# Performance work log

Measured on AMD Instinct MI355X. Metric: run time of the kernel, lower is better.

## Reference

```python
import jax, jax.numpy as jnp
import numpy as np

N = 65536
NUM_NODES = 100000
NUM_SAMPLED = 16
EMB = 128


def setup_inputs() -> dict:
    key = jax.random.key(0)
    k1, k2, k3, k4, k5 = jax.random.split(key, 5)
    inputs = {
        "input": jax.random.normal(k1, (N,), dtype=jnp.float32),
        "embs": jax.random.normal(k2, (N, EMB), dtype=jnp.float32),
        "label": jax.random.randint(k3, (N,), 0, NUM_NODES),
        "negs": jax.random.randint(k4, (N, NUM_SAMPLED), 0, NUM_NODES),
        # weights initialized ~ N(0, 1/sqrt(emb)) as in reset_parameters
        "weights": jax.random.normal(k5, (NUM_NODES, EMB), dtype=jnp.float32)
        * (1.0 / np.sqrt(EMB)),
    }
    return inputs


def reference(input, embs, label, negs, weights):
    n = input.shape[0]
    # positive term: log(sigmoid(<embs_i, weights[label_i]>))
    pos_score = jnp.sum(embs * weights[label], axis=1)  # [n]
    log_target = jax.nn.log_sigmoid(pos_score)
    # negative term: noise = -weights[negs]; bmm(noise, embs) -> [n, num_sampled]
    neg_score = -jnp.einsum("nkd,nd->nk", weights[negs], embs)
    sum_log_sampled = jnp.sum(jax.nn.log_sigmoid(neg_score), axis=1)  # [n]
    loss = log_target + sum_log_sampled
    return -jnp.sum(loss) / n
```

## Files before the change

### kernel.cpp

```cpp
#include <hip/hip_runtime.h>

#define NROWS 65536
#define EMB 128
#define NS 16
#define NUM_NODES 100000
#define HALF_NODE 50000
#define NB (NROWS / 16)
#define NB_F32 (NROWS / 16)

#define QSTEP 0.0296101f
#define QSTEP_INV 33.7722f
#define ESCALE 23.0f
#define SCALE (QSTEP / ESCALE)

__device__ __forceinline__ float log_sigmoid(float x) {
    return fminf(x, 0.0f) - __logf(1.0f + __expf(-fabsf(x)));
}

__device__ __forceinline__ int sdot4_sw(unsigned a, unsigned b, int c) {
#pragma unroll
    for (int i = 0; i < 4; ++i) {
        int ai = (int)(a << (24 - 8 * i)) >> 24;
        int bi = (int)(b << (24 - 8 * i)) >> 24;
        c += ai * bi;
    }
    return c;
}
#if defined(__has_builtin)
#if __has_builtin(__builtin_amdgcn_sdot4)
#define SDOT4(a, b, c) __builtin_amdgcn_sdot4((int)(a), (int)(b), (c), false)
#endif
#endif
#ifndef SDOT4
#define SDOT4(a, b, c) sdot4_sw((a), (b), (c))
#endif

#define DOTB(P, PE, PO, OUT)                                   \
    {                                                          \
        unsigned _b0 = (P) & 0x0F0F0F0Fu;                      \
        unsigned _b1 = ((P) >> 4) & 0x0F0F0F0Fu;               \
        OUT = SDOT4(_b1, (PO), SDOT4(_b0, (PE), 0));           \
    }

#define BFLYI(OUT, LO, HI, B, MASK)                   \
    {                                                 \
        int _k = (B) ? (HI) : (LO);                   \
        int _s = (B) ? (LO) : (HI);                   \
        OUT = _k + __shfl_xor(_s, (MASK), 64);        \
    }

__device__ __forceinline__ int qe8(float x) {
    int v = (int)rintf(x * ESCALE);
    return v < -127 ? -127 : (v > 127 ? 127 : v);
}

__global__ __launch_bounds__(256) void convert_w_i4(
    const float* __restrict__ w, unsigned int* __restrict__ out, int n8)
{
    int i = blockIdx.x * blockDim.x + threadIdx.x;
    if (i < n8) {
        const float4* p4 = (const float4*)(w + (size_t)i * 8);
        float4 a = p4[0], b = p4[1];
        float v[8] = {a.x, a.y, a.z, a.w, b.x, b.y, b.z, b.w};
        unsigned int p = 0;
#pragma unroll
        for (int j = 0; j < 8; ++j) {
            int n = (int)rintf(v[j] * QSTEP_INV);
            n = n < -7 ? -7 : (n > 7 ? 7 : n);
            p |= ((unsigned int)(n + 8)) << (4 * j);
        }
        out[i] = p;
    }
}

__device__ __forceinline__ float row_term_par(
    int row, int q, unsigned pbit,
    const int* __restrict__ label,
    const int* __restrict__ negs,
    const unsigned* __restrict__ wq,
    unsigned pe, unsigned po, int es)
{
    const int lab = label[row];
    const int4* ng = (const int4*)negs + (unsigned)row * 4u;
    const int4 n0 = ng[0], n1 = ng[1], n2 = ng[2], n3 = ng[3];

#define OWN(IDX) ((unsigned)((IDX) >= HALF_NODE) == pbit)
#define GATHER(IDX) (OWN(IDX) ? wq[(unsigned)(IDX) * 16u + (unsigned)q] : 0u)
    const unsigned wp0  = GATHER(n0.x), wp1  = GATHER(n0.y);
    const unsigned wp2  = GATHER(n0.z), wp3  = GATHER(n0.w);
    const unsigned wp4  = GATHER(n1.x), wp5  = GATHER(n1.y);
    const unsigned wp6  = GATHER(n1.z), wp7  = GATHER(n1.w);
    const unsigned wp8  = GATHER(n2.x), wp9  = GATHER(n2.y);
    const unsigned wp10 = GATHER(n2.z), wp11 = GATHER(n2.w);
    const unsigned wp12 = GATHER(n3.x), wp13 = GATHER(n3.y);
    const unsigned wp14 = GATHER(n3.z), wp15 = GATHER(n3.w);
    const unsigned wpp  = GATHER(lab);
#undef GATHER

    int a0, a1, a2, a3, a4, a5, a6, a7, a8, a9, a10, a11, a12, a13, a14, a15, posi;
    DOTB(wp0,  pe, po, a0);   DOTB(wp1,  pe, po, a1);
    DOTB(wp2,  pe, po, a2);   DOTB(wp3,  pe, po, a3);
    DOTB(wp4,  pe, po, a4);   DOTB(wp5,  pe, po, a5);
    DOTB(wp6,  pe, po, a6);   DOTB(wp7,  pe, po, a7);
    DOTB(wp8,  pe, po, a8);   DOTB(wp9,  pe, po, a9);
    DOTB(wp10, pe, po, a10);  DOTB(wp11, pe, po, a11);
    DOTB(wp12, pe, po, a12);  DOTB(wp13, pe, po, a13);
    DOTB(wp14, pe, po, a14);  DOTB(wp15, pe, po, a15);
    DOTB(wpp,  pe, po, posi);

    const bool b0 = (q & 1), b1 = (q & 2), b2 = (q & 4), b3 = (q & 8);
    int s10, s11, s12, s13, s14, s15, s16, s17;
    BFLYI(s10, a0,  a1,  b0, 1);  BFLYI(s11, a2,  a3,  b0, 1);
    BFLYI(s12, a4,  a5,  b0, 1);  BFLYI(s13, a6,  a7,  b0, 1);
    BFLYI(s14, a8,  a9,  b0, 1);  BFLYI(s15, a10, a11, b0, 1);
    BFLYI(s16, a12, a13, b0, 1);  BFLYI(s17, a14, a15, b0, 1);
    int s20, s21, s22, s23;
    BFLYI(s20, s10, s11, b1, 2);  BFLYI(s21, s12, s13, b1, 2);
    BFLYI(s22, s14, s15, b1, 2);  BFLYI(s23, s16, s17, b1, 2);
    int s30, s31;
    BFLYI(s30, s20, s21, b2, 4);  BFLYI(s31, s22, s23, b2, 4);
    int mynegi;
    BFLYI(mynegi, s30, s31, b3, 8);

    posi += __shfl_xor(posi, 1, 64);
    posi += __shfl_xor(posi, 2, 64);
    posi += __shfl_xor(posi, 4, 64);
    posi += __shfl_xor(posi, 8, 64);

    int mi = n0.x;
    mi = (q == 1)  ? n0.y : mi;  mi = (q == 2)  ? n0.z : mi;
    mi = (q == 3)  ? n0.w : mi;  mi = (q == 4)  ? n1.x : mi;
    mi = (q == 5)  ? n1.y : mi;  mi = (q == 6)  ? n1.z : mi;
    mi = (q == 7)  ? n1.w : mi;  mi = (q == 8)  ? n2.x : mi;
    mi = (q == 9)  ? n2.y : mi;  mi = (q == 10) ? n2.z : mi;
    mi = (q == 11) ? n2.w : mi;  mi = (q == 12) ? n3.x : mi;
    mi = (q == 13) ? n3.y : mi;  mi = (q == 14) ? n3.z : mi;
    mi = (q == 15) ? n3.w : mi;

    const int corr = es << 3;
    const float myneg = (float)(mynegi - corr) * SCALE;
    const float pos   = (float)(posi   - corr) * SCALE;

    float c = OWN(mi) ? log_sigmoid(-myneg) : 0.0f;
    if (q == 0 && OWN(lab)) c += log_sigmoid(pos);
#undef OWN

    c += __shfl_xor(c, 1, 64);
    c += __shfl_xor(c, 2, 64);
    c += __shfl_xor(c, 4, 64);
    c += __shfl_xor(c, 8, 64);
    return c;
}

__global__ __launch_bounds__(256) void nsloss_partial_i4(
    const float*        __restrict__ embs,
    const int*          __restrict__ label,
    const int*          __restrict__ negs,
    const unsigned int* __restrict__ wq,
    float*              __restrict__ partial)
{
    const int tid = threadIdx.x;
    const int q   = tid & 15;
    const int g   = tid >> 4;
    const unsigned bid  = blockIdx.x;
    const unsigned pbit = bid & 1u;
    const int base = (int)(bid >> 1) * 32;

    const float4* e8 = (const float4*)embs;
    float c = 0.0f;

#pragma unroll
    for (int rr = 0; rr < 2; ++rr) {
        const int row = base + rr * 16 + g;
        const unsigned eb4 = (unsigned)row * 32u;
        const float4 ea = e8[eb4 + 2u * q];
        const float4 eb = e8[eb4 + 2u * q + 1u];
        const int q0 = qe8(ea.x), q1 = qe8(ea.y), q2 = qe8(ea.z), q3 = qe8(ea.w);
        const int q4 = qe8(eb.x), q5 = qe8(eb.y), q6 = qe8(eb.z), q7 = qe8(eb.w);
        const unsigned pe = (unsigned)(q0 & 255) | ((unsigned)(q2 & 255) << 8) |
                            ((unsigned)(q4 & 255) << 16) | ((unsigned)(q6 & 255) << 24);
        const unsigned po = (unsigned)(q1 & 255) | ((unsigned)(q3 & 255) << 8) |
                            ((unsigned)(q5 & 255) << 16) | ((unsigned)(q7 & 255) << 24);
        int es = SDOT4(0x01010101u, pe, SDOT4(0x01010101u, po, 0));
        es += __shfl_xor(es, 1, 64);
        es += __shfl_xor(es, 2, 64);
        es += __shfl_xor(es, 4, 64);
        es += __shfl_xor(es, 8, 64);

        c += row_term_par(row, q, pbit, label, negs, wq, pe, po, es);
    }

    __shared__ float s[16];
    if (q == 0) s[g] = c;
    __syncthreads();
    if (tid == 0) {
        float t = 0.0f;
#pragma unroll
        for (int i = 0; i < 16; ++i) t += s[i];
        partial[bid] = t;
    }
}

__device__ __forceinline__ float dot8f(float4 a0, float4 a1, float4 b0, float4 b1) {
    return a0.x * b0.x + a0.y * b0.y + a0.z * b0.z + a0.w * b0.w +
           a1.x * b1.x + a1.y * b1.y + a1.z * b1.z + a1.w * b1.w;
}

__global__ __launch_bounds__(256) void nsloss_partial_f32(
    const float* __restrict__ embs,
    const int*   __restrict__ label,
    const int*   __restrict__ negs,
    const float* __restrict__ weights,
    float*       __restrict__ partial)
{
    const int tid = threadIdx.x;
    const int q   = tid & 15;
    const int row = blockIdx.x * 16 + (tid >> 4);

    const float4* e4 = (const float4*)(embs + (size_t)row * EMB);
    const float4 e0 = e4[q];
    const float4 e1 = e4[q + 16];

    const int lab = label[row];
    const int4* ng = (const int4*)(negs + (size_t)row * NS);
    const int4 n0 = ng[0], n1 = ng[1], n2 = ng[2], n3 = ng[3];
    const int nidx[NS] = {n0.x, n0.y, n0.z, n0.w, n1.x, n1.y, n1.z, n1.w,
                          n2.x, n2.y, n2.z, n2.w, n3.x, n3.y, n3.z, n3.w};

    float acc[NS + 1];
    {
        const float4* w4 = (const float4*)(weights + (size_t)lab * EMB);
        acc[NS] = dot8f(e0, e1, w4[q], w4[q + 16]);
    }
#pragma unroll
    for (int k = 0; k < NS; ++k) {
        const float4* w4 = (const float4*)(weights + (size_t)nidx[k] * EMB);
        acc[k] = dot8f(e0, e1, w4[q], w4[q + 16]);
    }

#pragma unroll
    for (int k = 0; k < NS + 1; ++k) {
        acc[k] += __shfl_xor(acc[k], 1, 64);
        acc[k] += __shfl_xor(acc[k], 2, 64);
        acc[k] += __shfl_xor(acc[k], 4, 64);
        acc[k] += __shfl_xor(acc[k], 8, 64);
    }

    float myneg = 0.0f;
#pragma unroll
    for (int k = 0; k < NS; ++k)
        if (q == k) myneg = acc[k];

    float cc = log_sigmoid(-myneg);
    if (q == 0) cc += log_sigmoid(acc[NS]);

    cc += __shfl_xor(cc, 1, 64);
    cc += __shfl_xor(cc, 2, 64);
    cc += __shfl_xor(cc, 4, 64);
    cc += __shfl_xor(cc, 8, 64);

    __shared__ float s[16];
    if (q == 0) s[tid >> 4] = cc;
    __syncthreads();
    if (tid == 0) {
        float t = 0.0f;
#pragma unroll
        for (int i = 0; i < 16; ++i) t += s[i];
        partial[blockIdx.x] = t;
    }
}

__global__ __launch_bounds__(1024) void nsloss_final(
    const float* __restrict__ partial,
    float*       __restrict__ out, int n)
{
    float v = 0.0f;
    for (int i = threadIdx.x; i < n; i += 1024) v += partial[i];
#pragma unroll
    for (int off = 32; off >= 1; off >>= 1) v += __shfl_xor(v, off, 64);

    __shared__ float s[16];
    if ((threadIdx.x & 63) == 0) s[threadIdx.x >> 6] = v;
    __syncthreads();
    if (threadIdx.x == 0) {
        float t = 0.0f;
#pragma unroll
        for (int i = 0; i < 16; ++i) t += s[i];
        out[0] = -t / (float)NROWS;
    }
}

extern "C" void kernel_launch(void* const* d_in, const int* in_sizes, int n_in,
                              void* d_out, int out_size, void* d_ws, size_t ws_size,
                              hipStream_t stream) {
    const float* embs    = (const float*)d_in[1];
    const int*   label   = (const int*)d_in[2];
    const int*   negs    = (const int*)d_in[3];
    const float* weights = (const float*)d_in[4];
    float* out = (float*)d_out;

    const size_t tbl_bytes = (size_t)NUM_NODES * EMB / 2;

    if (ws_size >= tbl_bytes + NB * sizeof(float)) {
        unsigned int* wq = (unsigned int*)d_ws;
        float* partial = (float*)((unsigned char*)d_ws + tbl_bytes);

        const int n8 = NUM_NODES * EMB / 8;
        convert_w_i4<<<(n8 + 255) / 256, 256, 0, stream>>>(weights, wq, n8);
        nsloss_partial_i4<<<NB, 256, 0, stream>>>(embs, label, negs, wq, partial);
        nsloss_final<<<1, 1024, 0, stream>>>(partial, out, NB);
    } else {
        float* partial = (float*)d_ws;
        nsloss_partial_f32<<<NB_F32, 256, 0, stream>>>(embs, label, negs, weights, partial);
        nsloss_final<<<1, 1024, 0, stream>>>(partial, out, NB_F32);
    }
}
```

Baseline: 41.32 us.

## Process both table halves per block with barrier-separated gather phases

Before this change, each block pair split the weight table by node-index half, and every row was handled twice across two blocks. Now each block handles its 32 rows alone. It gathers the low-half rows first, then passes a __syncthreads and a scheduling barrier before gathering the high-half rows, so all blocks work on the same half of the table at the same time to keep cache locality. This halves the number of blocks and removes the duplicated embedding load, quantisation and index loads per row. The cost is an extra barrier inside the row loop and less parallelism across blocks.

Result: faster. 38.67 us (-6.4%).

```diff
diff --git a/kernel.cpp b/kernel.cpp
--- a/kernel.cpp
+++ b/kernel.cpp
@@ -4,9 +4,9 @@
 #define EMB 128
 #define NS 16
 #define NUM_NODES 100000
-#define HALF_NODE 50000
-#define NB (NROWS / 16)
-#define NB_F32 (NROWS / 16)
+#define HALF_NODE 50000u
+#define NB (NROWS / 32)
+#define NB_R8 (NROWS / 16)
 
 #define QSTEP 0.0296101f
 #define QSTEP_INV 33.7722f
@@ -54,59 +54,90 @@
     return v < -127 ? -127 : (v > 127 ? 127 : v);
 }
 
-__global__ __launch_bounds__(256) void convert_w_i4(
-    const float* __restrict__ w, unsigned int* __restrict__ out, int n8)
-{
-    int i = blockIdx.x * blockDim.x + threadIdx.x;
-    if (i < n8) {
-        const float4* p4 = (const float4*)(w + (size_t)i * 8);
-        float4 a = p4[0], b = p4[1];
-        float v[8] = {a.x, a.y, a.z, a.w, b.x, b.y, b.z, b.w};
-        unsigned int p = 0;
-#pragma unroll
-        for (int j = 0; j < 8; ++j) {
-            int n = (int)rintf(v[j] * QSTEP_INV);
-            n = n < -7 ? -7 : (n > 7 ? 7 : n);
-            p |= ((unsigned int)(n + 8)) << (4 * j);
-        }
-        out[i] = p;
-    }
-}
-
-__device__ __forceinline__ float row_term_par(
-    int row, int q, unsigned pbit,
-    const int* __restrict__ label,
-    const int* __restrict__ negs,
-    const unsigned* __restrict__ wq,
-    unsigned pe, unsigned po, int es)
+__device__ __forceinline__ unsigned pack_w8(const float* __restrict__ w, unsigned i) {
+    const float4* p4 = (const float4*)(w + (size_t)i * 8);
+    float4 a = p4[0], b = p4[1];
+    float v[8] = {a.x, a.y, a.z, a.w, b.x, b.y, b.z, b.w};
+    unsigned p = 0;
+#pragma unroll
+    for (int j = 0; j < 8; ++j) {
+        int n = (int)rintf(v[j] * QSTEP_INV);
+        n = n < -7 ? -7 : (n > 7 ? 7 : n);
+        p |= ((unsigned)(n + 8)) << (4 * j);
+    }
+    return p;
+}
+
+__device__ __forceinline__ void pack_e(float4 ea, float4 eb,
+                                       unsigned& pe, unsigned& po, int& es)
+{
+    const int q0 = qe8(ea.x), q1 = qe8(ea.y), q2 = qe8(ea.z), q3 = qe8(ea.w);
+    const int q4 = qe8(eb.x), q5 = qe8(eb.y), q6 = qe8(eb.z), q7 = qe8(eb.w);
+    pe = (unsigned)(q0 & 255) | ((unsigned)(q2 & 255) << 8) |
+         ((unsigned)(q4 & 255) << 16) | ((unsigned)(q6 & 255) << 24);
+    po = (unsigned)(q1 & 255) | ((unsigned)(q3 & 255) << 8) |
+         ((unsigned)(q5 & 255) << 16) | ((unsigned)(q7 & 255) << 24);
+    int e = SDOT4(0x01010101u, pe, SDOT4(0x01010101u, po, 0));
+    e += __shfl_xor(e, 1, 64);
+    e += __shfl_xor(e, 2, 64);
+    e += __shfl_xor(e, 4, 64);
+    e += __shfl_xor(e, 8, 64);
+    es = e;
+}
+
+__device__ __forceinline__ float row_term_2p(int row, int q,
+                                             const int* __restrict__ label,
+                                             const int* __restrict__ negs,
+                                             const unsigned* __restrict__ wq,
+                                             unsigned pe, unsigned po, int es)
 {
     const int lab = label[row];
     const int4* ng = (const int4*)negs + (unsigned)row * 4u;
     const int4 n0 = ng[0], n1 = ng[1], n2 = ng[2], n3 = ng[3];
 
-#define OWN(IDX) ((unsigned)((IDX) >= HALF_NODE) == pbit)
-#define GATHER(IDX) (OWN(IDX) ? wq[(unsigned)(IDX) * 16u + (unsigned)q] : 0u)
-    const unsigned wp0  = GATHER(n0.x), wp1  = GATHER(n0.y);
-    const unsigned wp2  = GATHER(n0.z), wp3  = GATHER(n0.w);
-    const unsigned wp4  = GATHER(n1.x), wp5  = GATHER(n1.y);
-    const unsigned wp6  = GATHER(n1.z), wp7  = GATHER(n1.w);
-    const unsigned wp8  = GATHER(n2.x), wp9  = GATHER(n2.y);
-    const unsigned wp10 = GATHER(n2.z), wp11 = GATHER(n2.w);
-    const unsigned wp12 = GATHER(n3.x), wp13 = GATHER(n3.y);
-    const unsigned wp14 = GATHER(n3.z), wp15 = GATHER(n3.w);
-    const unsigned wpp  = GATHER(lab);
-#undef GATHER
-
     int a0, a1, a2, a3, a4, a5, a6, a7, a8, a9, a10, a11, a12, a13, a14, a15, posi;
-    DOTB(wp0,  pe, po, a0);   DOTB(wp1,  pe, po, a1);
-    DOTB(wp2,  pe, po, a2);   DOTB(wp3,  pe, po, a3);
-    DOTB(wp4,  pe, po, a4);   DOTB(wp5,  pe, po, a5);
-    DOTB(wp6,  pe, po, a6);   DOTB(wp7,  pe, po, a7);
-    DOTB(wp8,  pe, po, a8);   DOTB(wp9,  pe, po, a9);
-    DOTB(wp10, pe, po, a10);  DOTB(wp11, pe, po, a11);
-    DOTB(wp12, pe, po, a12);  DOTB(wp13, pe, po, a13);
-    DOTB(wp14, pe, po, a14);  DOTB(wp15, pe, po, a15);
-    DOTB(wpp,  pe, po, posi);
+
+    {
+#define GA(IDX) (((unsigned)(IDX) < HALF_NODE) ? wq[(unsigned)(IDX) * 16u + (unsigned)q] : 0u)
+        const unsigned w0  = GA(n0.x), w1  = GA(n0.y), w2  = GA(n0.z), w3  = GA(n0.w);
+        const unsigned w4  = GA(n1.x), w5  = GA(n1.y), w6  = GA(n1.z), w7  = GA(n1.w);
+        const unsigned w8  = GA(n2.x), w9  = GA(n2.y), w10 = GA(n2.z), w11 = GA(n2.w);
+        const unsigned w12 = GA(n3.x), w13 = GA(n3.y), w14 = GA(n3.z), w15 = GA(n3.w);
+        const unsigned wp  = GA(lab);
+#undef GA
+        DOTB(w0,  pe, po, a0);   DOTB(w1,  pe, po, a1);
+        DOTB(w2,  pe, po, a2);   DOTB(w3,  pe, po, a3);
+        DOTB(w4,  pe, po, a4);   DOTB(w5,  pe, po, a5);
+        DOTB(w6,  pe, po, a6);   DOTB(w7,  pe, po, a7);
+        DOTB(w8,  pe, po, a8);   DOTB(w9,  pe, po, a9);
+        DOTB(w10, pe, po, a10);  DOTB(w11, pe, po, a11);
+        DOTB(w12, pe, po, a12);  DOTB(w13, pe, po, a13);
+        DOTB(w14, pe, po, a14);  DOTB(w15, pe, po, a15);
+        DOTB(wp,  pe, po, posi);
+    }
+
+    __syncthreads();
+    __builtin_amdgcn_sched_barrier(0);
+
+    {
+#define GB(IDX) (((unsigned)(IDX) >= HALF_NODE) ? wq[(unsigned)(IDX) * 16u + (unsigned)q] : 0u)
+        const unsigned w0  = GB(n0.x), w1  = GB(n0.y), w2  = GB(n0.z), w3  = GB(n0.w);
+        const unsigned w4  = GB(n1.x), w5  = GB(n1.y), w6  = GB(n1.z), w7  = GB(n1.w);
+        const unsigned w8  = GB(n2.x), w9  = GB(n2.y), w10 = GB(n2.z), w11 = GB(n2.w);
+        const unsigned w12 = GB(n3.x), w13 = GB(n3.y), w14 = GB(n3.z), w15 = GB(n3.w);
+        const unsigned wp  = GB(lab);
+#undef GB
+        int b;
+        DOTB(w0,  pe, po, b); a0  += b;  DOTB(w1,  pe, po, b); a1  += b;
+        DOTB(w2,  pe, po, b); a2  += b;  DOTB(w3,  pe, po, b); a3  += b;
+        DOTB(w4,  pe, po, b); a4  += b;  DOTB(w5,  pe, po, b); a5  += b;
+        DOTB(w6,  pe, po, b); a6  += b;  DOTB(w7,  pe, po, b); a7  += b;
+        DOTB(w8,  pe, po, b); a8  += b;  DOTB(w9,  pe, po, b); a9  += b;
+        DOTB(w10, pe, po, b); a10 += b;  DOTB(w11, pe, po, b); a11 += b;
+        DOTB(w12, pe, po, b); a12 += b;  DOTB(w13, pe, po, b); a13 += b;
+        DOTB(w14, pe, po, b); a14 += b;  DOTB(w15, pe, po, b); a15 += b;
+        DOTB(wp,  pe, po, b); posi += b;
+    }
 
     const bool b0 = (q & 1), b1 = (q & 2), b2 = (q & 4), b3 = (q & 8);
     int s10, s11, s12, s13, s14, s15, s16, s17;
@@ -127,29 +158,25 @@
     posi += __shfl_xor(posi, 4, 64);
     posi += __shfl_xor(posi, 8, 64);
 
-    int mi = n0.x;
-    mi = (q == 1)  ? n0.y : mi;  mi = (q == 2)  ? n0.z : mi;
-    mi = (q == 3)  ? n0.w : mi;  mi = (q == 4)  ? n1.x : mi;
-    mi = (q == 5)  ? n1.y : mi;  mi = (q == 6)  ? n1.z : mi;
-    mi = (q == 7)  ? n1.w : mi;  mi = (q == 8)  ? n2.x : mi;
-    mi = (q == 9)  ? n2.y : mi;  mi = (q == 10) ? n2.z : mi;
-    mi = (q == 11) ? n2.w : mi;  mi = (q == 12) ? n3.x : mi;
-    mi = (q == 13) ? n3.y : mi;  mi = (q == 14) ? n3.z : mi;
-    mi = (q == 15) ? n3.w : mi;
-
     const int corr = es << 3;
     const float myneg = (float)(mynegi - corr) * SCALE;
     const float pos   = (float)(posi   - corr) * SCALE;
 
-    float c = OWN(mi) ? log_sigmoid(-myneg) : 0.0f;
-    if (q == 0 && OWN(lab)) c += log_sigmoid(pos);
-#undef OWN
+    float c = log_sigmoid(-myneg);
+    if (q == 0) c += log_sigmoid(pos);
 
     c += __shfl_xor(c, 1, 64);
     c += __shfl_xor(c, 2, 64);
     c += __shfl_xor(c, 4, 64);
     c += __shfl_xor(c, 8, 64);
     return c;
+}
+
+__global__ __launch_bounds__(256) void convert_w_i4(
+    const float* __restrict__ w, unsigned int* __restrict__ out, int n8)
+{
+    int i = blockIdx.x * blockDim.x + threadIdx.x;
+    if (i < n8) out[i] = pack_w8(w, (unsigned)i);
 }
 
 __global__ __launch_bounds__(256) void nsloss_partial_i4(
@@ -162,33 +189,29 @@
     const int tid = threadIdx.x;
     const int q   = tid & 15;
     const int g   = tid >> 4;
-    const unsigned bid  = blockIdx.x;
-    const unsigned pbit = bid & 1u;
-    const int base = (int)(bid >> 1) * 32;
+    const int row0 = blockIdx.x * 32 + g;
+    const int row1 = row0 + 16;
 
     const float4* e8 = (const float4*)embs;
-    float c = 0.0f;
-
-#pragma unroll
-    for (int rr = 0; rr < 2; ++rr) {
-        const int row = base + rr * 16 + g;
-        const unsigned eb4 = (unsigned)row * 32u;
-        const float4 ea = e8[eb4 + 2u * q];
-        const float4 eb = e8[eb4 + 2u * q + 1u];
-        const int q0 = qe8(ea.x), q1 = qe8(ea.y), q2 = qe8(ea.z), q3 = qe8(ea.w);
-        const int q4 = qe8(eb.x), q5 = qe8(eb.y), q6 = qe8(eb.z), q7 = qe8(eb.w);
-        const unsigned pe = (unsigned)(q0 & 255) | ((unsigned)(q2 & 255) << 8) |
-                            ((unsigned)(q4 & 255) << 16) | ((unsigned)(q6 & 255) << 24);
-        const unsigned po = (unsigned)(q1 & 255) | ((unsigned)(q3 & 255) << 8) |
-                            ((unsigned)(q5 & 255) << 16) | ((unsigned)(q7 & 255) << 24);
-        int es = SDOT4(0x01010101u, pe, SDOT4(0x01010101u, po, 0));
-        es += __shfl_xor(es, 1, 64);
-        es += __shfl_xor(es, 2, 64);
-        es += __shfl_xor(es, 4, 64);
-        es += __shfl_xor(es, 8, 64);
-
-        c += row_term_par(row, q, pbit, label, negs, wq, pe, po, es);
-    }
+    const unsigned eb0 = (unsigned)row0 * 32u;
+    const unsigned eb1 = (unsigned)row1 * 32u;
+
+    const float4 ea0 = e8[eb0 + 2u * q];
+    const float4 eb0v = e8[eb0 + 2u * q + 1u];
+    const float4 ea1 = e8[eb1 + 2u * q];
+    const float4 eb1v = e8[eb1 + 2u * q + 1u];
+
+    unsigned pe0, po0;
+    int es0;
+    pack_e(ea0, eb0v, pe0, po0, es0);
+
+    float c = row_term_2p(row0, q, label, negs, wq, pe0, po0, es0);
+
+    unsigned pe1, po1;
+    int es1;
+    pack_e(ea1, eb1v, pe1, po1, es1);
+
+    c += row_term_2p(row1, q, label, negs, wq, pe1, po1, es1);
 
     __shared__ float s[16];
     if (q == 0) s[g] = c;
@@ -197,7 +220,27 @@
         float t = 0.0f;
 #pragma unroll
         for (int i = 0; i < 16; ++i) t += s[i];
-        partial[bid] = t;
+        partial[blockIdx.x] = t;
+    }
+}
+
+__global__ __launch_bounds__(1024) void nsloss_final(
+    const float* __restrict__ partial,
+    float*       __restrict__ out, int n)
+{
+    float v = 0.0f;
+    for (int i = threadIdx.x; i < n; i += 1024) v += partial[i];
+#pragma unroll
+    for (int off = 32; off >= 1; off >>= 1) v += __shfl_xor(v, off, 64);
+
+    __shared__ float s[16];
+    if ((threadIdx.x & 63) == 0) s[threadIdx.x >> 6] = v;
+    __syncthreads();
+    if (threadIdx.x == 0) {
+        float t = 0.0f;
+#pragma unroll
+        for (int i = 0; i < 16; ++i) t += s[i];
+        out[0] = -t / (float)NROWS;
     }
 }
 
@@ -267,26 +310,6 @@
 #pragma unroll
         for (int i = 0; i < 16; ++i) t += s[i];
         partial[blockIdx.x] = t;
-    }
-}
-
-__global__ __launch_bounds__(1024) void nsloss_final(
-    const float* __restrict__ partial,
-    float*       __restrict__ out, int n)
-{
-    float v = 0.0f;
-    for (int i = threadIdx.x; i < n; i += 1024) v += partial[i];
-#pragma unroll
-    for (int off = 32; off >= 1; off >>= 1) v += __shfl_xor(v, off, 64);
-
-    __shared__ float s[16];
-    if ((threadIdx.x & 63) == 0) s[threadIdx.x >> 6] = v;
-    __syncthreads();
-    if (threadIdx.x == 0) {
-        float t = 0.0f;
-#pragma unroll
-        for (int i = 0; i < 16; ++i) t += s[i];
-        out[0] = -t / (float)NROWS;
     }
 }
 
@@ -311,7 +334,7 @@
         nsloss_final<<<1, 1024, 0, stream>>>(partial, out, NB);
     } else {
         float* partial = (float*)d_ws;
-        nsloss_partial_f32<<<NB_F32, 256, 0, stream>>>(embs, label, negs, weights, partial);
-        nsloss_final<<<1, 1024, 0, stream>>>(partial, out, NB_F32);
-    }
-}
+        nsloss_partial_f32<<<NB_R8, 256, 0, stream>>>(embs, label, negs, weights, partial);
+        nsloss_final<<<1, 1024, 0, stream>>>(partial, out, NB_R8);
+    }
+}
```
